# Kernel optimization log

Hardware: AMD Instinct MI355X
Metric: run time of the kernel (lower is better)

Reference implementation:

```python
import jax, jax.numpy as jnp
import numpy as np


def setup_inputs() -> dict:
    key = jax.random.key(0)
    ks = jax.random.split(key, 8)
    bs, G, A, C, CM, D, H = 256, 169, 3, 5, 32, 1024, 512
    return {
        "boxes_sml0": jax.random.uniform(ks[0], (bs, G, A, C), dtype=jnp.float32),
        "masks_in0": jax.random.normal(ks[1], (bs, G, A, CM), dtype=jnp.float32),
        "feat": jax.random.normal(ks[2], (bs, D, 13, 13), dtype=jnp.float32),
        "lang_feat": jax.random.normal(ks[3], (bs, H), dtype=jnp.float32),
        "W_vs": jax.random.normal(ks[4], (D, H), dtype=jnp.float32) * 0.02,
        "b_vs": jnp.zeros((H,), dtype=jnp.float32),
        "W_ts": jax.random.normal(ks[5], (H, H), dtype=jnp.float32) * 0.02,
        "b_ts": jnp.zeros((H,), dtype=jnp.float32),
        "select_num": 32,
    }


def reference(boxes_sml0, masks_in0, feat, lang_feat, W_vs, b_vs, W_ts, b_ts, select_num):
    bs, G, A, C = boxes_sml0.shape
    CM = masks_in0.shape[-1]
    D = feat.shape[1]

    # mean over anchors of objectness channel 4 -> top-k grid selection
    mean_score = jnp.mean(boxes_sml0[..., 4], axis=2)           # [bs, G]
    _, idx = jax.lax.top_k(mean_score, select_num)              # [bs, k]

    # scatter-mask + masked_select in torch == gather of selected grids
    boxes_new = jnp.take_along_axis(boxes_sml0, idx[:, :, None, None], axis=1)  # [bs,k,A,C]
    masks_new = jnp.take_along_axis(masks_in0, idx[:, :, None, None], axis=1)   # [bs,k,A,CM]

    # gather visual features of selected grids, project
    i_all = feat.reshape(bs, D, -1).transpose(0, 2, 1)          # [bs, G, D]
    i_sel = jnp.take_along_axis(i_all, idx[:, :, None], axis=1) # [bs, k, D]
    x_new = i_sel @ W_vs + b_vs                                 # [bs, k, H]
    y_new = lang_feat @ W_ts + b_ts                             # [bs, H]

    # head: visual-text similarity, pick top grid per batch
    sim = jnp.einsum('bkh,bh->bk', x_new, y_new)                # [bs, k]
    maxval = jnp.max(sim, axis=1)                               # [bs]
    pred = jnp.argmax(sim, axis=1)                              # [bs]

    sel_b = jnp.take_along_axis(boxes_new, pred[:, None, None, None], axis=1)[:, 0]  # [bs,A,C]
    sel_m = jnp.take_along_axis(masks_new, pred[:, None, None, None], axis=1)[:, 0]  # [bs,A,CM]

    # cxcywh -> xyxy with original in-place overwrite semantics
    cx, cy, w, h = sel_b[..., 0], sel_b[..., 1], sel_b[..., 2], sel_b[..., 3]
    x1 = cx - w / 2
    y1 = cy - h / 2
    x2 = x1 + w
    y2 = y1 + h
    refined = jnp.concatenate(
        [jnp.stack([x1, y1, x2, y2], axis=-1), sel_b[..., 4:]], axis=-1)  # [bs,A,C]

    # pick anchor with max objectness, gather 5-dim box and mask coeffs
    aidx = jnp.argmax(refined[..., 4], axis=1)                  # [bs]
    box_new = jnp.take_along_axis(refined[..., :5], aidx[:, None, None], axis=1)  # [bs,1,5]
    mask_new = jnp.take_along_axis(sel_m, aidx[:, None, None], axis=1)            # [bs,1,CM]
    return box_new, mask_new, maxval
```

## Files before the change

kernel.cpp:

```cpp
#include <hip/hip_runtime.h>
#include <cfloat>
#include <cstdint>

#define GBM 64
#define GBN 64
#define GBK 64
#define GPAD 68

#define G_    169
#define D_    1024
#define H_    512
#define NW    8
#define ROWG  8
#define NGRP  16
#define GRPF  1352
#define NV    338
#define NBUF  3
#define SPL   8

typedef unsigned int u32;

__device__ __forceinline__ void gload_lds16(const float* g, float* l) {
    __builtin_amdgcn_global_load_lds(
        (const __attribute__((address_space(1))) u32*)g,
        (__attribute__((address_space(3))) u32*)l, 16, 0, 0);
}

__device__ __forceinline__ void stage_group(const float* gsrc, float* ldsbase, int lane) {
    #pragma unroll
    for (int j = 0; j < 6; j++) {
        int idx = j * 64 + lane;
        if (idx < NV)
            gload_lds16(gsrc + 4 * idx, ldsbase + j * 256);
    }
}

__global__ __launch_bounds__(256) void gemm_splitk(
    const float* __restrict__ A, const float* __restrict__ B,
    float* __restrict__ Cpart, int M, int N, int K)
{
    __shared__ __align__(16) float Asm[GBK][GPAD];
    __shared__ __align__(16) float Bsm[GBK][GPAD];
    int t  = threadIdx.x;
    int m0 = blockIdx.y * GBM, n0 = blockIdx.x * GBN;
    int ks = blockIdx.z * GBK;

    #pragma unroll
    for (int i = 0; i < 4; i++) {
        int v = t + 256 * i;
        int m = v >> 4, k4 = (v & 15) * 4;
        float4 x = *(const float4*)&A[(size_t)(m0 + m) * K + ks + k4];
        Asm[k4 + 0][m] = x.x; Asm[k4 + 1][m] = x.y;
        Asm[k4 + 2][m] = x.z; Asm[k4 + 3][m] = x.w;
    }
    #pragma unroll
    for (int i = 0; i < 4; i++) {
        int v = t + 256 * i;
        int r = v >> 4, c4 = (v & 15) * 4;
        *(float4*)&Bsm[r][c4] = *(const float4*)&B[(size_t)(ks + r) * N + n0 + c4];
    }
    __syncthreads();

    int r4 = (t >> 4) * 4, c4 = (t & 15) * 4;
    float acc[4][4] = {{0.f}};
    #pragma unroll
    for (int kk = 0; kk < GBK; kk++) {
        float4 a = *(const float4*)&Asm[kk][r4];
        float4 b = *(const float4*)&Bsm[kk][c4];
        float av[4] = {a.x, a.y, a.z, a.w};
        float bv[4] = {b.x, b.y, b.z, b.w};
        #pragma unroll
        for (int i = 0; i < 4; i++)
            #pragma unroll
            for (int j = 0; j < 4; j++) acc[i][j] += av[i] * bv[j];
    }
    float* Cp = Cpart + (size_t)blockIdx.z * M * N;
    #pragma unroll
    for (int i = 0; i < 4; i++) {
        float4 v = {acc[i][0], acc[i][1], acc[i][2], acc[i][3]};
        *(float4*)&Cp[(size_t)(m0 + r4 + i) * N + n0 + c4] = v;
    }
}

__global__ __launch_bounds__(512) void feat_final(
    const float* __restrict__ feat, const float* __restrict__ py,
    const float* __restrict__ W_vs,
    const float* __restrict__ boxes, const float* __restrict__ masks,
    const float* __restrict__ b_ts, const float* __restrict__ b_vs,
    const int* __restrict__ kptr,
    float* __restrict__ out_box, float* __restrict__ out_mask,
    float* __restrict__ out_max,
    int bs, int AN, int CH, int CM)
{
    __shared__ __align__(16) float buf[NW][NBUF][GRPF];
    __shared__ __align__(16) float ys[H_];
    __shared__ float accw[NW * 176];
    __shared__ float simall[176];
    __shared__ float ms[176];
    __shared__ int   selg[176];
    __shared__ float simv[176];
    __shared__ float redw[NW];
    __shared__ float bbs;
    __shared__ int   selp[2];

    const int b = blockIdx.x;
    const int t = threadIdx.x;
    const int w = t >> 6, lane = t & 63;

    {
        float yv = b_ts[t];
        #pragma unroll
        for (int s = 0; s < SPL; s++) yv += py[((size_t)s * bs + b) * H_ + t];
        ys[t] = yv;
    }
    __syncthreads();

    float4 yreg[16];
    #pragma unroll
    for (int j = 0; j < 16; j++)
        yreg[j] = *(const float4*)&ys[(lane & 7) * 4 + j * 32];

    const float* gsrc = feat + ((size_t)b * D_ + (size_t)w * 128) * G_;
    stage_group(gsrc,        buf[w][0], lane);
    stage_group(gsrc + GRPF, buf[w][1], lane);

    float acc0 = 0.f, acc1 = 0.f, acc2 = 0.f;
    const bool g2 = lane < (G_ - 128);
    for (int gi = 0; gi < NGRP; gi++) {
        const float* Wp = W_vs + (size_t)(w * 128 + gi * 8 + (lane >> 3)) * H_;
        float4 wr[16];
        #pragma unroll
        for (int j = 0; j < 16; j++)
            wr[j] = *(const float4*)&Wp[(lane & 7) * 4 + j * 32];
        __builtin_amdgcn_sched_barrier(0);
        if (gi + 2 < NGRP)
            stage_group(gsrc + (size_t)(gi + 2) * GRPF, buf[w][(gi + 2) % NBUF], lane);
        __builtin_amdgcn_sched_barrier(0);
        if (gi + 2 < NGRP)
            asm volatile("s_waitcnt vmcnt(6)" ::: "memory");
        else
            asm volatile("s_waitcnt vmcnt(0)" ::: "memory");
        __builtin_amdgcn_sched_barrier(0);

        float zpart = 0.f;
        #pragma unroll
        for (int j = 0; j < 16; j++)
            zpart += wr[j].x * yreg[j].x + wr[j].y * yreg[j].y
                   + wr[j].z * yreg[j].z + wr[j].w * yreg[j].w;
        zpart += __shfl_xor(zpart, 1);
        zpart += __shfl_xor(zpart, 2);
        zpart += __shfl_xor(zpart, 4);

        const float* bp = buf[w][gi % NBUF];
        #pragma unroll
        for (int r = 0; r < ROWG; r++) {
            float zv = __shfl(zpart, r << 3, 64);
            acc0 += bp[r * G_ + lane] * zv;
            acc1 += bp[r * G_ + lane + 64] * zv;
            if (g2) acc2 += bp[r * G_ + lane + 128] * zv;
        }
    }
    accw[w * 176 + lane]      = acc0;
    accw[w * 176 + lane + 64] = acc1;
    if (g2) accw[w * 176 + lane + 128] = acc2;
    __syncthreads();

    int k = *kptr; if (k > G_) k = G_;

    if (t < G_) {
        float s = 0.f;
        #pragma unroll
        for (int ww = 0; ww < NW; ww++) s += accw[ww * 176 + t];
        simall[t] = s;
        const float* bp = boxes + (size_t)(b * G_ + t) * AN * CH;
        float o = 0.f;
        for (int a = 0; a < AN; a++) o += bp[a * CH + 4];
        ms[t] = o / (float)AN;
    }
    {
        float part = b_vs[t] * ys[t];
        #pragma unroll
        for (int off = 32; off > 0; off >>= 1) part += __shfl_down(part, off);
        if (lane == 0) redw[w] = part;
    }
    __syncthreads();
    if (t == 0) {
        float s = 0.f;
        #pragma unroll
        for (int ww = 0; ww < NW; ww++) s += redw[ww];
        bbs = s;
    }

    if (t < G_) {
        float mv = ms[t];
        int rank = 0;
        for (int g = 0; g < G_; g++) {
            float o = ms[g];
            rank += (int)((o > mv) | ((o == mv) & (g < t)));
        }
        if (rank < k) selg[rank] = t;
    }
    __syncthreads();

    if (t < k) simv[t] = simall[selg[t]];
    __syncthreads();

    if (t == 0) {
        float best = -FLT_MAX; int br = 0;
        for (int r = 0; r < k; r++) if (simv[r] > best) { best = simv[r]; br = r; }
        int gs = selg[br];
        const float* bp = boxes + (size_t)(b * G_ + gs) * AN * CH;
        float bo = -FLT_MAX; int ai = 0;
        for (int a = 0; a < AN; a++) { float o = bp[a * CH + 4]; if (o > bo) { bo = o; ai = a; } }
        float cx = bp[ai * CH + 0], cy = bp[ai * CH + 1];
        float ww = bp[ai * CH + 2], hh = bp[ai * CH + 3];
        float x1 = cx - ww * 0.5f, y1 = cy - hh * 0.5f;
        out_box[(size_t)b * CH + 0] = x1;
        out_box[(size_t)b * CH + 1] = y1;
        out_box[(size_t)b * CH + 2] = x1 + ww;
        out_box[(size_t)b * CH + 3] = y1 + hh;
        for (int c = 4; c < CH; c++) out_box[(size_t)b * CH + c] = bp[ai * CH + c];
        out_max[b] = best + bbs;
        selp[0] = gs; selp[1] = ai;
    }
    __syncthreads();
    if (t < CM) {
        out_mask[(size_t)b * CM + t] =
            masks[((size_t)(b * G_ + selp[0]) * AN + selp[1]) * CM + t];
    }
}

extern "C" void kernel_launch(void* const* d_in, const int* in_sizes, int n_in,
                              void* d_out, int out_size, void* d_ws, size_t ws_size,
                              hipStream_t stream)
{
    const float* boxes = (const float*)d_in[0];
    const float* masks = (const float*)d_in[1];
    const float* feat  = (const float*)d_in[2];
    const float* lang  = (const float*)d_in[3];
    const float* W_vs  = (const float*)d_in[4];
    const float* b_vs  = (const float*)d_in[5];
    const float* W_ts  = (const float*)d_in[6];
    const float* b_ts  = (const float*)d_in[7];
    const int*   kptr  = (const int*)d_in[8];

    int H  = in_sizes[5];
    int bs = in_sizes[3] / H;
    int AN = 3;
    int CH = in_sizes[0] / (bs * G_ * AN);
    int CM = in_sizes[1] / (bs * G_ * AN);

    float* py = (float*)d_ws;

    float* out_box  = (float*)d_out;
    float* out_mask = out_box + (size_t)bs * CH;
    float* out_max  = out_mask + (size_t)bs * CM;

    dim3 g1(H / GBN, bs / GBM, SPL);
    gemm_splitk<<<g1, 256, 0, stream>>>(lang, W_ts, py, bs, H, H);
    feat_final<<<bs, 512, 0, stream>>>(feat, py, W_vs, boxes, masks, b_ts, b_vs,
                                       kptr, out_box, out_mask, out_max,
                                       bs, AN, CH, CM);
}
```

Baseline: 56.48 us.

## Double-buffer W_vs register loads across groups and read y from LDS

The W_vs row loads for the next group are issued one iteration ahead into a second register buffer, so their latency overlaps the current group's compute. The vmcnt waits are retuned to count both the W loads and the feat LDS staging loads. The y vector is now read from LDS inside the loop instead of being held in registers, which frees registers for the second buffer. Launch bounds request two blocks per CU, which caps register use and risks spills; the full unroll also makes the hand-counted vmcnt values fragile.

```diff
diff --git a/kernel.cpp b/kernel.cpp
--- a/kernel.cpp
+++ b/kernel.cpp
@@ -82,7 +82,7 @@
     }
 }
 
-__global__ __launch_bounds__(512) void feat_final(
+__global__ __launch_bounds__(512, 2) void feat_final(
     const float* __restrict__ feat, const float* __restrict__ py,
     const float* __restrict__ W_vs,
     const float* __restrict__ boxes, const float* __restrict__ masks,
@@ -115,38 +115,45 @@
     }
     __syncthreads();
 
-    float4 yreg[16];
+    const int ylo  = (lane & 7) * 4;
+    const int wrow = lane >> 3;
+    const float* gsrc  = feat + ((size_t)b * D_ + (size_t)w * 128) * G_;
+    const float* Wbase = W_vs + ((size_t)(w * 128 + wrow)) * H_ + ylo;
+
+    float4 wr[2][16];
     #pragma unroll
     for (int j = 0; j < 16; j++)
-        yreg[j] = *(const float4*)&ys[(lane & 7) * 4 + j * 32];
-
-    const float* gsrc = feat + ((size_t)b * D_ + (size_t)w * 128) * G_;
+        wr[0][j] = *(const float4*)&Wbase[j * 32];
     stage_group(gsrc,        buf[w][0], lane);
     stage_group(gsrc + GRPF, buf[w][1], lane);
 
     float acc0 = 0.f, acc1 = 0.f, acc2 = 0.f;
     const bool g2 = lane < (G_ - 128);
+    #pragma unroll
     for (int gi = 0; gi < NGRP; gi++) {
-        const float* Wp = W_vs + (size_t)(w * 128 + gi * 8 + (lane >> 3)) * H_;
-        float4 wr[16];
-        #pragma unroll
-        for (int j = 0; j < 16; j++)
-            wr[j] = *(const float4*)&Wp[(lane & 7) * 4 + j * 32];
-        __builtin_amdgcn_sched_barrier(0);
+        if (gi + 1 < NGRP) {
+            const float* Wp = Wbase + (size_t)(gi + 1) * 8 * H_;
+            #pragma unroll
+            for (int j = 0; j < 16; j++)
+                wr[(gi + 1) & 1][j] = *(const float4*)&Wp[j * 32];
+        }
         if (gi + 2 < NGRP)
             stage_group(gsrc + (size_t)(gi + 2) * GRPF, buf[w][(gi + 2) % NBUF], lane);
-        __builtin_amdgcn_sched_barrier(0);
-        if (gi + 2 < NGRP)
-            asm volatile("s_waitcnt vmcnt(6)" ::: "memory");
+        if (gi + 3 <= NGRP)
+            asm volatile("s_waitcnt vmcnt(28)" ::: "memory");
+        else if (gi + 2 == NGRP)
+            asm volatile("s_waitcnt vmcnt(22)" ::: "memory");
         else
             asm volatile("s_waitcnt vmcnt(0)" ::: "memory");
         __builtin_amdgcn_sched_barrier(0);
 
         float zpart = 0.f;
         #pragma unroll
-        for (int j = 0; j < 16; j++)
-            zpart += wr[j].x * yreg[j].x + wr[j].y * yreg[j].y
-                   + wr[j].z * yreg[j].z + wr[j].w * yreg[j].w;
+        for (int j = 0; j < 16; j++) {
+            float4 yv = *(const float4*)&ys[ylo + j * 32];
+            float4 wv = wr[gi & 1][j];
+            zpart += wv.x * yv.x + wv.y * yv.y + wv.z * yv.z + wv.w * yv.w;
+        }
         zpart += __shfl_xor(zpart, 1);
         zpart += __shfl_xor(zpart, 2);
         zpart += __shfl_xor(zpart, 4);
```

Result: slower. 132.9 us (+135.3%).
